# Kernel optimization log

Hardware: AMD Instinct MI355X
Metric: run time of the kernel (lower is better)

The kernel has to match this reference:

```python
import jax, jax.numpy as jnp
import numpy as np

B, S, D, H = 4, 2048, 1024, 16
HD = D // H


def setup_inputs() -> dict:
    key = jax.random.key(0)
    k1, k2, k3 = jax.random.split(key, 3)
    x = jax.random.normal(k1, (B, S, D), dtype=jnp.float32)
    # xavier-ish scaling for stable softmax
    W_attn = jax.random.normal(k2, (3 * D, D), dtype=jnp.float32) * (1.0 / np.sqrt(2 * D))
    b_attn = jnp.zeros((3 * D,), dtype=jnp.float32)
    W_out = jax.random.normal(k3, (D, D), dtype=jnp.float32) * (1.0 / np.sqrt(D))
    b_out = jnp.zeros((D,), dtype=jnp.float32)
    return {"x": x, "W_attn": W_attn, "b_attn": b_attn, "W_out": W_out, "b_out": b_out}


def reference(x, W_attn, b_attn, W_out, b_out):
    bs, seq, d = x.shape
    # fused QKV projection (torch Linear: y = x @ W.T + b)
    kqv = jnp.einsum("bsd,ed->bse", x, W_attn) + b_attn
    # NOTE: source splits as k, q, v (k first)
    k, q, v = jnp.split(kqv, 3, axis=2)
    # [b, s, h, hd] -> [b, h, s, hd]
    k = k.reshape(bs, seq, H, HD).transpose(0, 2, 1, 3)
    q = q.reshape(bs, seq, H, HD).transpose(0, 2, 1, 3)
    v = v.reshape(bs, seq, H, HD).transpose(0, 2, 1, 3)
    scale = 1.0 / np.sqrt(HD)
    scores = jnp.einsum("bhqd,bhkd->bhqk", q, k) * scale
    attn = jax.nn.softmax(scores, axis=-1)
    y = jnp.einsum("bhqk,bhkd->bhqd", attn, v)
    y = y.transpose(0, 2, 1, 3).reshape(bs, seq, d)
    out = jnp.einsum("bsd,ed->bse", y, W_out) + b_out
    return out
```

## Files before the change

### kernel.cpp

```cpp
#include <hip/hip_runtime.h>

typedef unsigned short u16;
typedef unsigned int u32;
typedef __attribute__((ext_vector_type(2))) u32 u32x2;
typedef __attribute__((ext_vector_type(4))) u32 u32x4;
typedef __attribute__((ext_vector_type(8))) short bf16x8;
typedef __attribute__((ext_vector_type(4))) short bf16x4;
typedef __attribute__((ext_vector_type(4))) float f32x4;

__device__ __forceinline__ u16 f2bf(float f) {
  u32 b = __float_as_uint(f);
  b += 0x7fffu + ((b >> 16) & 1u);
  return (u16)(b >> 16);
}

__device__ __forceinline__ u32 pk2bf(float a, float b) {
#if __has_builtin(__builtin_amdgcn_cvt_pk_bf16_f32)
  return __builtin_bit_cast(u32, __builtin_amdgcn_cvt_pk_bf16_f32(a, b));
#else
  return (u32)f2bf(a) | ((u32)f2bf(b) << 16);
#endif
}

__device__ __forceinline__ bf16x8 mk_ones8() {
  u32x4 t;
  t[0] = t[1] = t[2] = t[3] = 0x3F803F80u;
  return __builtin_bit_cast(bf16x8, t);
}

__device__ __forceinline__ float fexp2(float x) {
#if __has_builtin(__builtin_amdgcn_exp2f)
  return __builtin_amdgcn_exp2f(x);
#else
  return exp2f(x);
#endif
}

__device__ __forceinline__ void gload_lds16(const u16* g, u16* l) {
  __builtin_amdgcn_global_load_lds((const __attribute__((address_space(1))) void*)g,
                                   (__attribute__((address_space(3))) void*)l, 16, 0, 0);
}

__global__ __launch_bounds__(256) void cvt_f32_bf16(const float* __restrict__ in,
                                                    u16* __restrict__ out) {
  long i = ((long)blockIdx.x * 256 + threadIdx.x) * 8;
  u32 u[8];
#pragma unroll
  for (int j = 0; j < 8; j++) {
    u32 b = __float_as_uint(in[i + j]);
    u[j] = (b + 0x7fffu + ((b >> 16) & 1u)) >> 16;
  }
  u32x4 o;
  o[0] = u[0] | (u[1] << 16);
  o[1] = u[2] | (u[3] << 16);
  o[2] = u[4] | (u[5] << 16);
  o[3] = u[6] | (u[7] << 16);
  *(u32x4*)(out + i) = o;
}

__device__ __forceinline__ void gemm_core_128(const u16* __restrict__ A,
                                              const u16* __restrict__ B, int K,
                                              int m0, int n0, u16* As, u16* Bs,
                                              f32x4 acc[4][4]) {
  int t = threadIdx.x;
  int lane = t & 63, w = t >> 6;
  int quad = lane >> 4, l16 = lane & 15;
  int wm = (w >> 1) * 64, wn = (w & 1) * 64;
  int lr = lane >> 3, lc = lane & 7;
  int cg = lc ^ lr;
  int swz = l16 & 7;
  for (int k0 = 0; k0 < K; k0 += 64) {
#pragma unroll
    for (int i = 0; i < 4; i++) {
      int r0 = i * 32 + w * 8;
      gload_lds16(&A[(long)(m0 + r0 + lr) * K + k0 + cg * 8], &As[r0 * 64]);
      gload_lds16(&B[(long)(n0 + r0 + lr) * K + k0 + cg * 8], &Bs[r0 * 64]);
    }
    __syncthreads();
#pragma unroll
    for (int ks = 0; ks < 2; ks++) {
      bf16x8 a[4], b[4];
#pragma unroll
      for (int tm = 0; tm < 4; tm++)
        a[tm] = *(const bf16x8*)&As[(wm + tm * 16 + l16) * 64 + ((ks * 4 + quad) ^ swz) * 8];
#pragma unroll
      for (int tn = 0; tn < 4; tn++)
        b[tn] = *(const bf16x8*)&Bs[(wn + tn * 16 + l16) * 64 + ((ks * 4 + quad) ^ swz) * 8];
#pragma unroll
      for (int tm = 0; tm < 4; tm++)
#pragma unroll
        for (int tn = 0; tn < 4; tn++)
          acc[tm][tn] = __builtin_amdgcn_mfma_f32_16x16x32_bf16(a[tm], b[tn],
                                                                acc[tm][tn], 0, 0, 0);
    }
    __syncthreads();
  }
}

#define QSCALE 0.1803368801f
__global__ __launch_bounds__(256) void gemm_qkv(const u16* __restrict__ A,
                                                const u16* __restrict__ B,
                                                const float* __restrict__ bias,
                                                u16* __restrict__ Kg,
                                                u16* __restrict__ Qg,
                                                u16* __restrict__ Vg) {
  __shared__ __align__(16) u16 As[128 * 64];
  __shared__ __align__(16) u16 Bs[128 * 64];
  const int K = 1024;
  int m0 = blockIdx.y * 128, n0 = blockIdx.x * 128;
  f32x4 acc[4][4];
#pragma unroll
  for (int i = 0; i < 4; i++)
#pragma unroll
    for (int j = 0; j < 4; j++) acc[i][j] = (f32x4)0.0f;
  gemm_core_128(A, B, K, m0, n0, As, Bs, acc);

  int t = threadIdx.x, lane = t & 63, w = t >> 6;
  int quad = lane >> 4, l16 = lane & 15;
  int wm = (w >> 1) * 64, wn = (w & 1) * 64;
#pragma unroll
  for (int tn = 0; tn < 4; tn++) {
    int n = n0 + wn + tn * 16 + l16;
    float bv = bias[n];
    int which = n >> 10;
    int h = (n >> 6) & 15, d = n & 63;
#pragma unroll
    for (int tm = 0; tm < 4; tm++) {
      int m = m0 + wm + tm * 16 + quad * 4;
      int b = m >> 11, s = m & 2047;
      long bh = (long)b * 16 + h;
      if (which == 2) {
        u32x2 pk;
        pk[0] = pk2bf(acc[tm][tn][0] + bv, acc[tm][tn][1] + bv);
        pk[1] = pk2bf(acc[tm][tn][2] + bv, acc[tm][tn][3] + bv);
        *(u32x2*)&Vg[(bh * 64 + d) * 2048 + s] = pk;
      } else {
#pragma unroll
        for (int r = 0; r < 4; r++) {
          float v = acc[tm][tn][r] + bv;
          if (which == 0)
            Kg[(bh * 2048 + s + r) * 64 + d] = f2bf(v);
          else
            Qg[(bh * 2048 + s + r) * 64 + d] = f2bf(v * QSCALE);
        }
      }
    }
  }
}

__global__ __launch_bounds__(256) void gemm_out(const u16* __restrict__ A,
                                                const u16* __restrict__ B,
                                                const float* __restrict__ bias,
                                                float* __restrict__ out) {
  __shared__ __align__(16) u16 As[128 * 64];
  __shared__ __align__(16) u16 Bs[128 * 64];
  const int K = 1024, N = 1024;
  int m0 = blockIdx.y * 128, n0 = blockIdx.x * 128;
  f32x4 acc[4][4];
#pragma unroll
  for (int i = 0; i < 4; i++)
#pragma unroll
    for (int j = 0; j < 4; j++) acc[i][j] = (f32x4)0.0f;
  gemm_core_128(A, B, K, m0, n0, As, Bs, acc);

  int t = threadIdx.x, lane = t & 63, w = t >> 6;
  int quad = lane >> 4, l16 = lane & 15;
  int wm = (w >> 1) * 64, wn = (w & 1) * 64;
#pragma unroll
  for (int tn = 0; tn < 4; tn++) {
    int n = n0 + wn + tn * 16 + l16;
    float bv = bias[n];
#pragma unroll
    for (int tm = 0; tm < 4; tm++) {
#pragma unroll
      for (int r = 0; r < 4; r++) {
        int m = m0 + wm + tm * 16 + quad * 4 + r;
        out[(long)m * N + n] = acc[tm][tn][r] + bv;
      }
    }
  }
}

#define SYNC                                       \
  __builtin_amdgcn_sched_barrier(0);               \
  asm volatile("s_waitcnt vmcnt(0)" ::: "memory"); \
  __builtin_amdgcn_s_barrier();                    \
  __builtin_amdgcn_sched_barrier(0)

#define STAGE_KV(tt, bb)                                      \
  do {                                                        \
    gload_lds16(Kst + (long)(tt)*4096, &Ks[bb][w * 8 * 64]);  \
    gload_lds16(Vst + (tt)*64, &Vs[bb][w * 8 * 64]);          \
  } while (0)

#define COMPUTE(bb)                                                            \
  do {                                                                         \
    bf16x8 pf_[2][2];                                                          \
    _Pragma("unroll") for (int tq = 0; tq < 2; tq++) {                         \
      f32x4 s_[4];                                                             \
      __builtin_amdgcn_s_setprio(1);                                           \
      _Pragma("unroll") for (int tn = 0; tn < 4; tn++) {                       \
        bf16x8 kf0 = *(const bf16x8*)(kL0 + (bb)*4096 + tn * 1024);            \
        bf16x8 kf1 = *(const bf16x8*)(kL1 + (bb)*4096 + tn * 1024);            \
        s_[tn] = __builtin_amdgcn_mfma_f32_16x16x32_bf16(kf0, qf[tq][0], Z,    \
                                                         0, 0, 0);             \
        s_[tn] = __builtin_amdgcn_mfma_f32_16x16x32_bf16(kf1, qf[tq][1],       \
                                                         s_[tn], 0, 0, 0);     \
      }                                                                        \
      __builtin_amdgcn_s_setprio(0);                                           \
      _Pragma("unroll") for (int tn = 0; tn < 4; tn++) {                       \
        float e0 = fexp2(s_[tn][0]);                                           \
        float e1 = fexp2(s_[tn][1]);                                           \
        float e2 = fexp2(s_[tn][2]);                                           \
        float e3 = fexp2(s_[tn][3]);                                           \
        u32x2 pk;                                                              \
        pk[0] = pk2bf(e0, e1);                                                 \
        pk[1] = pk2bf(e2, e3);                                                 \
        *(u32x2*)(pW + tq * 1024 + woff[tn]) = pk;                             \
      }                                                                        \
    }                                                                          \
    _Pragma("unroll") for (int ks = 0; ks < 2; ks++)                           \
        _Pragma("unroll") for (int tq = 0; tq < 2; tq++) {                     \
      u32x2 lo = *(const u32x2*)(pR + tq * 1024 + prlo[ks]);                   \
      u32x2 hi = *(const u32x2*)(pR + tq * 1024 + prhi[ks]);                   \
      u32x4 cc;                                                                \
      cc[0] = lo[0];                                                           \
      cc[1] = lo[1];                                                           \
      cc[2] = hi[0];                                                           \
      cc[3] = hi[1];                                                           \
      pf_[tq][ks] = __builtin_bit_cast(bf16x8, cc);                            \
    }                                                                          \
    __builtin_amdgcn_s_setprio(1);                                             \
    _Pragma("unroll") for (int ks = 0; ks < 2; ks++) {                         \
      acc_sum[0] = __builtin_amdgcn_mfma_f32_16x16x32_bf16(ONES, pf_[0][ks],   \
                                                           acc_sum[0], 0, 0, 0); \
      acc_sum[1] = __builtin_amdgcn_mfma_f32_16x16x32_bf16(ONES, pf_[1][ks],   \
                                                           acc_sum[1], 0, 0, 0); \
      _Pragma("unroll") for (int dt = 0; dt < 4; dt++) {                       \
        bf16x8 vf = *(const bf16x8*)(vL[ks] + (bb)*4096 + dt * 1024);          \
        acc[dt][0] = __builtin_amdgcn_mfma_f32_16x16x32_bf16(vf, pf_[0][ks],   \
                                                             acc[dt][0], 0, 0, 0); \
        acc[dt][1] = __builtin_amdgcn_mfma_f32_16x16x32_bf16(vf, pf_[1][ks],   \
                                                             acc[dt][1], 0, 0, 0); \
      }                                                                        \
    }                                                                          \
    __builtin_amdgcn_s_setprio(0);                                             \
  } while (0)

__global__ __launch_bounds__(512, 4) void attn_kernel(const u16* __restrict__ Qg,
                                                      const u16* __restrict__ Kg,
                                                      const u16* __restrict__ Vg,
                                                      u16* __restrict__ Y) {
  __shared__ __align__(16) u16 Ks[2][64 * 64];
  __shared__ __align__(16) u16 Vs[2][64 * 64];
  __shared__ __align__(16) u16 Ps[8 * 32 * 64];
  int t = threadIdx.x, lane = t & 63, w = t >> 6;
  int quad = lane >> 4, l16 = lane & 15;
  int bh = blockIdx.y;
  int q0 = blockIdx.x * 256 + w * 32;
  int lr = lane >> 3, lc = lane & 7, cg = lc ^ lr;
  int swz = l16 & 7;
  u16* Pw = Ps + w * 2048;

  bf16x8 qf[2][2];
#pragma unroll
  for (int tq = 0; tq < 2; tq++) {
    const u16* qp = Qg + ((long)bh * 2048 + q0 + tq * 16 + l16) * 64;
    qf[tq][0] = *(const bf16x8*)(qp + quad * 8);
    qf[tq][1] = *(const bf16x8*)(qp + 32 + quad * 8);
  }

  const f32x4 Z = {0.0f, 0.0f, 0.0f, 0.0f};
  const bf16x8 ONES = mk_ones8();

  f32x4 acc[4][2];
  f32x4 acc_sum[2];
#pragma unroll
  for (int dt = 0; dt < 4; dt++)
#pragma unroll
    for (int tq = 0; tq < 2; tq++) acc[dt][tq] = (f32x4)0.0f;
  acc_sum[0] = (f32x4)0.0f;
  acc_sum[1] = (f32x4)0.0f;

  const u16* kL0 = &Ks[0][l16 * 64 + (quad ^ swz) * 8];
  const u16* kL1 = &Ks[0][l16 * 64 + ((4 + quad) ^ swz) * 8];
  const u16* vL[2] = {&Vs[0][l16 * 64 + (quad ^ swz) * 8],
                      &Vs[0][l16 * 64 + ((4 + quad) ^ swz) * 8]};
  u16* pW = Pw + l16 * 64;
  const u16* pR = Pw + l16 * 64;
  int woff[4], prlo[2], prhi[2];
#pragma unroll
  for (int tn = 0; tn < 4; tn++) woff[tn] = ((tn * 4 + quad) ^ l16) * 4;
#pragma unroll
  for (int ks = 0; ks < 2; ks++) {
    prlo[ks] = ((ks * 8 + quad * 2) ^ l16) * 4;
    prhi[ks] = ((ks * 8 + quad * 2 + 1) ^ l16) * 4;
  }

  const u16* Kst = Kg + ((long)bh * 2048 + w * 8 + lr) * 64 + cg * 8;
  const u16* Vst = Vg + ((long)(bh * 64 + w * 8 + lr)) * 2048 + cg * 8;

  STAGE_KV(0, 0);
  for (int tt = 0; tt < 30; tt += 2) {
    SYNC;
    STAGE_KV(tt + 1, 1);
    COMPUTE(0);
    SYNC;
    STAGE_KV(tt + 2, 0);
    COMPUTE(1);
  }
  SYNC;
  STAGE_KV(31, 1);
  COMPUTE(0);
  SYNC;
  COMPUTE(1);

  int b = bh >> 4, h = bh & 15;
#pragma unroll
  for (int tq = 0; tq < 2; tq++) {
    float inv = 1.0f / acc_sum[tq][0];
    long row = (long)b * 2048 + q0 + tq * 16 + l16;
#pragma unroll
    for (int dt = 0; dt < 4; dt++) {
      u32x2 pk;
      pk[0] = pk2bf(acc[dt][tq][0] * inv, acc[dt][tq][1] * inv);
      pk[1] = pk2bf(acc[dt][tq][2] * inv, acc[dt][tq][3] * inv);
      *(u32x2*)&Y[row * 1024 + h * 64 + dt * 16 + quad * 4] = pk;
    }
  }
}

extern "C" void kernel_launch(void* const* d_in, const int* in_sizes, int n_in,
                              void* d_out, int out_size, void* d_ws, size_t ws_size,
                              hipStream_t stream) {
  const float* x = (const float*)d_in[0];
  const float* W_attn = (const float*)d_in[1];
  const float* b_attn = (const float*)d_in[2];
  const float* W_out = (const float*)d_in[3];
  const float* b_out = (const float*)d_in[4];
  float* out = (float*)d_out;

  char* ws = (char*)d_ws;
  u16* xb = (u16*)ws;
  u16* Wab = (u16*)(ws + 16777216);
  u16* Wob = (u16*)(ws + 16777216 + 6291456);
  u16* Kg = (u16*)(ws + 25165824);
  u16* Qg = Kg + 8388608;
  u16* Vg = Qg + 8388608;
  u16* Yb = xb;

  cvt_f32_bf16<<<4096, 256, 0, stream>>>(x, xb);
  cvt_f32_bf16<<<1536, 256, 0, stream>>>(W_attn, Wab);
  cvt_f32_bf16<<<512, 256, 0, stream>>>(W_out, Wob);

  gemm_qkv<<<dim3(24, 64), 256, 0, stream>>>(xb, Wab, b_attn, Kg, Qg, Vg);
  attn_kernel<<<dim3(8, 64), 512, 0, stream>>>(Qg, Kg, Vg, Yb);
  gemm_out<<<dim3(8, 64), 256, 0, stream>>>(Yb, Wob, b_out, out);
}
```

Baseline: 292.7 us.

## Split attention KV tile across wave pairs with LDS reduction; fuse conversion kernels

The attention kernel now uses 256-thread blocks covering 64 queries instead of 512 threads covering 256 queries, launching four times as many blocks. Within each block, pairs of waves split each 64-key tile's columns and merge their partial outputs and row sums through LDS at the end. This is meant to raise the block count for better CU occupancy and load balance, at the cost of loading K/V four times more often per head and adding an epilogue reduction. The three f32-to-bf16 conversion launches are also merged into one kernel to cut launch overhead.

After: 287.4 us. No clear change (-1.8%).

```diff
diff --git a/kernel.cpp b/kernel.cpp
--- a/kernel.cpp
+++ b/kernel.cpp
@@ -5,7 +5,6 @@
 typedef __attribute__((ext_vector_type(2))) u32 u32x2;
 typedef __attribute__((ext_vector_type(4))) u32 u32x4;
 typedef __attribute__((ext_vector_type(8))) short bf16x8;
-typedef __attribute__((ext_vector_type(4))) short bf16x4;
 typedef __attribute__((ext_vector_type(4))) float f32x4;
 
 __device__ __forceinline__ u16 f2bf(float f) {
@@ -36,14 +35,33 @@
 #endif
 }
 
+__device__ __forceinline__ f32x4 mfma32(bf16x8 a, bf16x8 b, f32x4 c) {
+  return __builtin_amdgcn_mfma_f32_16x16x32_bf16(a, b, c, 0, 0, 0);
+}
+
 __device__ __forceinline__ void gload_lds16(const u16* g, u16* l) {
   __builtin_amdgcn_global_load_lds((const __attribute__((address_space(1))) void*)g,
                                    (__attribute__((address_space(3))) void*)l, 16, 0, 0);
 }
 
-__global__ __launch_bounds__(256) void cvt_f32_bf16(const float* __restrict__ in,
-                                                    u16* __restrict__ out) {
-  long i = ((long)blockIdx.x * 256 + threadIdx.x) * 8;
+__global__ __launch_bounds__(256) void cvt_all(const float* __restrict__ x,
+                                               const float* __restrict__ wa,
+                                               const float* __restrict__ wo,
+                                               u16* __restrict__ xb,
+                                               u16* __restrict__ wab,
+                                               u16* __restrict__ wob) {
+  int blk = blockIdx.x;
+  const float* in;
+  u16* out;
+  long base;
+  if (blk < 4096) {
+    in = x; out = xb; base = blk;
+  } else if (blk < 5632) {
+    in = wa; out = wab; base = blk - 4096;
+  } else {
+    in = wo; out = wob; base = blk - 5632;
+  }
+  long i = (base * 256 + threadIdx.x) * 8;
   u32 u[8];
 #pragma unroll
   for (int j = 0; j < 8; j++) {
@@ -187,28 +205,31 @@
   __builtin_amdgcn_s_barrier();                    \
   __builtin_amdgcn_sched_barrier(0)
 
-#define STAGE_KV(tt, bb)                                      \
-  do {                                                        \
-    gload_lds16(Kst + (long)(tt)*4096, &Ks[bb][w * 8 * 64]);  \
-    gload_lds16(Vst + (tt)*64, &Vs[bb][w * 8 * 64]);          \
+#define STAGE_KV(tt, bb)                                                       \
+  do {                                                                         \
+    gload_lds16(Kst + (long)(tt)*4096, Ks0 + (bb)*4096 + w * 1024);            \
+    gload_lds16(Kst + (long)(tt)*4096 + 512, Ks0 + (bb)*4096 + w * 1024 + 512);\
+    gload_lds16(Vst + (tt)*64, Vs0 + (bb)*4096 + w * 1024);                    \
+    gload_lds16(Vst + (tt)*64 + 8 * 2048, Vs0 + (bb)*4096 + w * 1024 + 512);   \
   } while (0)
 
 #define COMPUTE(bb)                                                            \
   do {                                                                         \
-    bf16x8 pf_[2][2];                                                          \
+    bf16x8 kf_[2][2];                                                          \
+    _Pragma("unroll") for (int tn = 0; tn < 2; tn++) {                         \
+      kf_[tn][0] = *(const bf16x8*)(kL0 + (bb)*4096 + tn * 1024);              \
+      kf_[tn][1] = *(const bf16x8*)(kL1 + (bb)*4096 + tn * 1024);              \
+    }                                                                          \
+    bf16x8 pf_[2];                                                             \
     _Pragma("unroll") for (int tq = 0; tq < 2; tq++) {                         \
-      f32x4 s_[4];                                                             \
+      f32x4 s_[2];                                                             \
       __builtin_amdgcn_s_setprio(1);                                           \
-      _Pragma("unroll") for (int tn = 0; tn < 4; tn++) {                       \
-        bf16x8 kf0 = *(const bf16x8*)(kL0 + (bb)*4096 + tn * 1024);            \
-        bf16x8 kf1 = *(const bf16x8*)(kL1 + (bb)*4096 + tn * 1024);            \
-        s_[tn] = __builtin_amdgcn_mfma_f32_16x16x32_bf16(kf0, qf[tq][0], Z,    \
-                                                         0, 0, 0);             \
-        s_[tn] = __builtin_amdgcn_mfma_f32_16x16x32_bf16(kf1, qf[tq][1],       \
-                                                         s_[tn], 0, 0, 0);     \
+      _Pragma("unroll") for (int tn = 0; tn < 2; tn++) {                       \
+        s_[tn] = mfma32(kf_[tn][0], qf[tq][0], Z);                             \
+        s_[tn] = mfma32(kf_[tn][1], qf[tq][1], s_[tn]);                        \
       }                                                                        \
       __builtin_amdgcn_s_setprio(0);                                           \
-      _Pragma("unroll") for (int tn = 0; tn < 4; tn++) {                       \
+      _Pragma("unroll") for (int tn = 0; tn < 2; tn++) {                       \
         float e0 = fexp2(s_[tn][0]);                                           \
         float e1 = fexp2(s_[tn][1]);                                           \
         float e2 = fexp2(s_[tn][2]);                                           \
@@ -216,51 +237,46 @@
         u32x2 pk;                                                              \
         pk[0] = pk2bf(e0, e1);                                                 \
         pk[1] = pk2bf(e2, e3);                                                 \
-        *(u32x2*)(pW + tq * 1024 + woff[tn]) = pk;                             \
+        *(u32x2*)(pW + tq * 512 + woff[tn]) = pk;                              \
       }                                                                        \
     }                                                                          \
-    _Pragma("unroll") for (int ks = 0; ks < 2; ks++)                           \
-        _Pragma("unroll") for (int tq = 0; tq < 2; tq++) {                     \
-      u32x2 lo = *(const u32x2*)(pR + tq * 1024 + prlo[ks]);                   \
-      u32x2 hi = *(const u32x2*)(pR + tq * 1024 + prhi[ks]);                   \
+    _Pragma("unroll") for (int tq = 0; tq < 2; tq++) {                         \
+      u32x2 lo = *(const u32x2*)(pR + tq * 512 + prlo);                        \
+      u32x2 hi = *(const u32x2*)(pR + tq * 512 + prhi);                        \
       u32x4 cc;                                                                \
       cc[0] = lo[0];                                                           \
       cc[1] = lo[1];                                                           \
       cc[2] = hi[0];                                                           \
       cc[3] = hi[1];                                                           \
-      pf_[tq][ks] = __builtin_bit_cast(bf16x8, cc);                            \
+      pf_[tq] = __builtin_bit_cast(bf16x8, cc);                                \
     }                                                                          \
     __builtin_amdgcn_s_setprio(1);                                             \
-    _Pragma("unroll") for (int ks = 0; ks < 2; ks++) {                         \
-      acc_sum[0] = __builtin_amdgcn_mfma_f32_16x16x32_bf16(ONES, pf_[0][ks],   \
-                                                           acc_sum[0], 0, 0, 0); \
-      acc_sum[1] = __builtin_amdgcn_mfma_f32_16x16x32_bf16(ONES, pf_[1][ks],   \
-                                                           acc_sum[1], 0, 0, 0); \
-      _Pragma("unroll") for (int dt = 0; dt < 4; dt++) {                       \
-        bf16x8 vf = *(const bf16x8*)(vL[ks] + (bb)*4096 + dt * 1024);          \
-        acc[dt][0] = __builtin_amdgcn_mfma_f32_16x16x32_bf16(vf, pf_[0][ks],   \
-                                                             acc[dt][0], 0, 0, 0); \
-        acc[dt][1] = __builtin_amdgcn_mfma_f32_16x16x32_bf16(vf, pf_[1][ks],   \
-                                                             acc[dt][1], 0, 0, 0); \
-      }                                                                        \
+    acc_sum[0] = mfma32(ONES, pf_[0], acc_sum[0]);                             \
+    acc_sum[1] = mfma32(ONES, pf_[1], acc_sum[1]);                             \
+    _Pragma("unroll") for (int dt = 0; dt < 4; dt++) {                         \
+      bf16x8 vf = *(const bf16x8*)(vL + (bb)*4096 + dt * 1024);                \
+      acc[dt][0] = mfma32(vf, pf_[0], acc[dt][0]);                             \
+      acc[dt][1] = mfma32(vf, pf_[1], acc[dt][1]);                             \
     }                                                                          \
     __builtin_amdgcn_s_setprio(0);                                             \
   } while (0)
 
-__global__ __launch_bounds__(512, 4) void attn_kernel(const u16* __restrict__ Qg,
+__global__ __launch_bounds__(256, 4) void attn_kernel(const u16* __restrict__ Qg,
                                                       const u16* __restrict__ Kg,
                                                       const u16* __restrict__ Vg,
                                                       u16* __restrict__ Y) {
-  __shared__ __align__(16) u16 Ks[2][64 * 64];
-  __shared__ __align__(16) u16 Vs[2][64 * 64];
-  __shared__ __align__(16) u16 Ps[8 * 32 * 64];
+  __shared__ __align__(16) u16 lds[20480];
+  u16* Ks0 = lds;
+  u16* Vs0 = lds + 8192;
+  u16* Ps0 = lds + 16384;
+
   int t = threadIdx.x, lane = t & 63, w = t >> 6;
   int quad = lane >> 4, l16 = lane & 15;
+  int p = w >> 1, kvh = w & 1;
   int bh = blockIdx.y;
-  int q0 = blockIdx.x * 256 + w * 32;
+  int q0 = blockIdx.x * 64 + p * 32;
   int lr = lane >> 3, lc = lane & 7, cg = lc ^ lr;
   int swz = l16 & 7;
-  u16* Pw = Ps + w * 2048;
 
   bf16x8 qf[2][2];
 #pragma unroll
@@ -282,23 +298,19 @@
   acc_sum[0] = (f32x4)0.0f;
   acc_sum[1] = (f32x4)0.0f;
 
-  const u16* kL0 = &Ks[0][l16 * 64 + (quad ^ swz) * 8];
-  const u16* kL1 = &Ks[0][l16 * 64 + ((4 + quad) ^ swz) * 8];
-  const u16* vL[2] = {&Vs[0][l16 * 64 + (quad ^ swz) * 8],
-                      &Vs[0][l16 * 64 + ((4 + quad) ^ swz) * 8]};
-  u16* pW = Pw + l16 * 64;
-  const u16* pR = Pw + l16 * 64;
-  int woff[4], prlo[2], prhi[2];
-#pragma unroll
-  for (int tn = 0; tn < 4; tn++) woff[tn] = ((tn * 4 + quad) ^ l16) * 4;
-#pragma unroll
-  for (int ks = 0; ks < 2; ks++) {
-    prlo[ks] = ((ks * 8 + quad * 2) ^ l16) * 4;
-    prhi[ks] = ((ks * 8 + quad * 2 + 1) ^ l16) * 4;
-  }
-
-  const u16* Kst = Kg + ((long)bh * 2048 + w * 8 + lr) * 64 + cg * 8;
-  const u16* Vst = Vg + ((long)(bh * 64 + w * 8 + lr)) * 2048 + cg * 8;
+  const u16* kL0 = Ks0 + (kvh * 32 + l16) * 64 + (quad ^ swz) * 8;
+  const u16* kL1 = Ks0 + (kvh * 32 + l16) * 64 + ((4 + quad) ^ swz) * 8;
+  const u16* vL = Vs0 + l16 * 64 + ((kvh * 4 + quad) ^ swz) * 8;
+  u16* pW = Ps0 + w * 1024 + l16 * 32;
+  const u16* pR = pW;
+  int woff[2];
+#pragma unroll
+  for (int tn = 0; tn < 2; tn++) woff[tn] = ((tn * 4 + quad) ^ swz) * 4;
+  int prlo = ((quad * 2) ^ swz) * 4;
+  int prhi = ((quad * 2 + 1) ^ swz) * 4;
+
+  const u16* Kst = Kg + ((long)bh * 2048 + w * 16 + lr) * 64 + cg * 8;
+  const u16* Vst = Vg + ((long)(bh * 64 + w * 16 + lr)) * 2048 + cg * 8;
 
   STAGE_KV(0, 0);
   for (int tt = 0; tt < 30; tt += 2) {
@@ -315,17 +327,35 @@
   SYNC;
   COMPUTE(1);
 
-  int b = bh >> 4, h = bh & 15;
-#pragma unroll
-  for (int tq = 0; tq < 2; tq++) {
-    float inv = 1.0f / acc_sum[tq][0];
-    long row = (long)b * 2048 + q0 + tq * 16 + l16;
-#pragma unroll
-    for (int dt = 0; dt < 4; dt++) {
-      u32x2 pk;
-      pk[0] = pk2bf(acc[dt][tq][0] * inv, acc[dt][tq][1] * inv);
-      pk[1] = pk2bf(acc[dt][tq][2] * inv, acc[dt][tq][3] * inv);
-      *(u32x2*)&Y[row * 1024 + h * 64 + dt * 16 + quad * 4] = pk;
+  __syncthreads();
+  float* red = (float*)lds;
+  int slot = (p * 64 + lane) * 44;
+  if (kvh) {
+#pragma unroll
+    for (int dt = 0; dt < 4; dt++)
+#pragma unroll
+      for (int tq = 0; tq < 2; tq++)
+        *(f32x4*)(red + slot + (dt * 2 + tq) * 4) = acc[dt][tq];
+    red[slot + 32] = acc_sum[0][0];
+    red[slot + 33] = acc_sum[1][0];
+  }
+  __syncthreads();
+  if (!kvh) {
+    float s0 = acc_sum[0][0] + red[slot + 32];
+    float s1 = acc_sum[1][0] + red[slot + 33];
+    float inv[2] = {1.0f / s0, 1.0f / s1};
+    int b = bh >> 4, h = bh & 15;
+#pragma unroll
+    for (int tq = 0; tq < 2; tq++) {
+      long row = (long)b * 2048 + q0 + tq * 16 + l16;
+#pragma unroll
+      for (int dt = 0; dt < 4; dt++) {
+        f32x4 a = acc[dt][tq] + *(const f32x4*)(red + slot + (dt * 2 + tq) * 4);
+        u32x2 pk;
+        pk[0] = pk2bf(a[0] * inv[tq], a[1] * inv[tq]);
+        pk[1] = pk2bf(a[2] * inv[tq], a[3] * inv[tq]);
+        *(u32x2*)&Y[row * 1024 + h * 64 + dt * 16 + quad * 4] = pk;
+      }
     }
   }
 }
@@ -349,11 +379,9 @@
   u16* Vg = Qg + 8388608;
   u16* Yb = xb;
 
-  cvt_f32_bf16<<<4096, 256, 0, stream>>>(x, xb);
-  cvt_f32_bf16<<<1536, 256, 0, stream>>>(W_attn, Wab);
-  cvt_f32_bf16<<<512, 256, 0, stream>>>(W_out, Wob);
+  cvt_all<<<6144, 256, 0, stream>>>(x, W_attn, W_out, xb, Wab, Wob);
 
   gemm_qkv<<<dim3(24, 64), 256, 0, stream>>>(xb, Wab, b_attn, Kg, Qg, Vg);
-  attn_kernel<<<dim3(8, 64), 512, 0, stream>>>(Qg, Kg, Vg, Yb);
+  attn_kernel<<<dim3(32, 64), 256, 0, stream>>>(Qg, Kg, Vg, Yb);
   gemm_out<<<dim3(8, 64), 256, 0, stream>>>(Yb, Wob, b_out, out);
 }
```

## Swap GEMM operand roles for vectorized epilogue stores and merge conversion kernels

Applied to the files above, without the earlier changes.

Both projection GEMMs now treat the weight matrix as the A operand and the activations as B, so the output tile is transposed. Each lane's four accumulator rows then map to contiguous feature indices, which allows packed 8-byte bf16 stores for K and Q and 16-byte float4 stores for the final output instead of scattered scalar stores. The V store turns into scalar strided writes, and the grid dimensions are swapped to match. The three fp32-to-bf16 conversion launches are also merged into one kernel to save launch overhead.

Result: faster. 278.3 us (-4.9%).

```diff
diff --git a/kernel.cpp b/kernel.cpp
--- a/kernel.cpp
+++ b/kernel.cpp
@@ -5,7 +5,6 @@
 typedef __attribute__((ext_vector_type(2))) u32 u32x2;
 typedef __attribute__((ext_vector_type(4))) u32 u32x4;
 typedef __attribute__((ext_vector_type(8))) short bf16x8;
-typedef __attribute__((ext_vector_type(4))) short bf16x4;
 typedef __attribute__((ext_vector_type(4))) float f32x4;
 
 __device__ __forceinline__ u16 f2bf(float f) {
@@ -41,9 +40,24 @@
                                    (__attribute__((address_space(3))) void*)l, 16, 0, 0);
 }
 
-__global__ __launch_bounds__(256) void cvt_f32_bf16(const float* __restrict__ in,
-                                                    u16* __restrict__ out) {
-  long i = ((long)blockIdx.x * 256 + threadIdx.x) * 8;
+__global__ __launch_bounds__(256) void cvt_all(const float* __restrict__ x,
+                                               const float* __restrict__ wa,
+                                               const float* __restrict__ wo,
+                                               u16* __restrict__ xb,
+                                               u16* __restrict__ wab,
+                                               u16* __restrict__ wob) {
+  int blk = blockIdx.x;
+  const float* in;
+  u16* out;
+  long base;
+  if (blk < 4096) {
+    in = x; out = xb; base = blk;
+  } else if (blk < 5632) {
+    in = wa; out = wab; base = blk - 4096;
+  } else {
+    in = wo; out = wob; base = blk - 5632;
+  }
+  long i = (base * 256 + threadIdx.x) * 8;
   u32 u[8];
 #pragma unroll
   for (int j = 0; j < 8; j++) {
@@ -118,31 +132,33 @@
   int t = threadIdx.x, lane = t & 63, w = t >> 6;
   int quad = lane >> 4, l16 = lane & 15;
   int wm = (w >> 1) * 64, wn = (w & 1) * 64;
-#pragma unroll
-  for (int tn = 0; tn < 4; tn++) {
-    int n = n0 + wn + tn * 16 + l16;
-    float bv = bias[n];
-    int which = n >> 10;
-    int h = (n >> 6) & 15, d = n & 63;
-#pragma unroll
-    for (int tm = 0; tm < 4; tm++) {
-      int m = m0 + wm + tm * 16 + quad * 4;
-      int b = m >> 11, s = m & 2047;
+  int which = m0 >> 10;
+#pragma unroll
+  for (int tm = 0; tm < 4; tm++) {
+    int m = m0 + wm + tm * 16 + quad * 4;
+    int h = (m >> 6) & 15, d0 = m & 63;
+    f32x4 b4 = *(const f32x4*)&bias[m];
+#pragma unroll
+    for (int tn = 0; tn < 4; tn++) {
+      int n = n0 + wn + tn * 16 + l16;
+      int b = n >> 11, s = n & 2047;
       long bh = (long)b * 16 + h;
-      if (which == 2) {
+      if (which == 0) {
         u32x2 pk;
-        pk[0] = pk2bf(acc[tm][tn][0] + bv, acc[tm][tn][1] + bv);
-        pk[1] = pk2bf(acc[tm][tn][2] + bv, acc[tm][tn][3] + bv);
-        *(u32x2*)&Vg[(bh * 64 + d) * 2048 + s] = pk;
+        pk[0] = pk2bf(acc[tm][tn][0] + b4[0], acc[tm][tn][1] + b4[1]);
+        pk[1] = pk2bf(acc[tm][tn][2] + b4[2], acc[tm][tn][3] + b4[3]);
+        *(u32x2*)&Kg[(bh * 2048 + s) * 64 + d0] = pk;
+      } else if (which == 1) {
+        u32x2 pk;
+        pk[0] = pk2bf((acc[tm][tn][0] + b4[0]) * QSCALE,
+                      (acc[tm][tn][1] + b4[1]) * QSCALE);
+        pk[1] = pk2bf((acc[tm][tn][2] + b4[2]) * QSCALE,
+                      (acc[tm][tn][3] + b4[3]) * QSCALE);
+        *(u32x2*)&Qg[(bh * 2048 + s) * 64 + d0] = pk;
       } else {
 #pragma unroll
-        for (int r = 0; r < 4; r++) {
-          float v = acc[tm][tn][r] + bv;
-          if (which == 0)
-            Kg[(bh * 2048 + s + r) * 64 + d] = f2bf(v);
-          else
-            Qg[(bh * 2048 + s + r) * 64 + d] = f2bf(v * QSCALE);
-        }
+        for (int r = 0; r < 4; r++)
+          Vg[(bh * 64 + d0 + r) * 2048 + s] = f2bf(acc[tm][tn][r] + b4[r]);
       }
     }
   }
@@ -154,7 +170,7 @@
                                                 float* __restrict__ out) {
   __shared__ __align__(16) u16 As[128 * 64];
   __shared__ __align__(16) u16 Bs[128 * 64];
-  const int K = 1024, N = 1024;
+  const int K = 1024;
   int m0 = blockIdx.y * 128, n0 = blockIdx.x * 128;
   f32x4 acc[4][4];
 #pragma unroll
@@ -167,16 +183,14 @@
   int quad = lane >> 4, l16 = lane & 15;
   int wm = (w >> 1) * 64, wn = (w & 1) * 64;
 #pragma unroll
-  for (int tn = 0; tn < 4; tn++) {
-    int n = n0 + wn + tn * 16 + l16;
-    float bv = bias[n];
-#pragma unroll
-    for (int tm = 0; tm < 4; tm++) {
-#pragma unroll
-      for (int r = 0; r < 4; r++) {
-        int m = m0 + wm + tm * 16 + quad * 4 + r;
-        out[(long)m * N + n] = acc[tm][tn][r] + bv;
-      }
+  for (int tm = 0; tm < 4; tm++) {
+    int m = m0 + wm + tm * 16 + quad * 4;
+    f32x4 b4 = *(const f32x4*)&bias[m];
+#pragma unroll
+    for (int tn = 0; tn < 4; tn++) {
+      int n = n0 + wn + tn * 16 + l16;
+      f32x4 o = acc[tm][tn] + b4;
+      *(f32x4*)&out[(long)n * 1024 + m] = o;
     }
   }
 }
@@ -349,11 +363,9 @@
   u16* Vg = Qg + 8388608;
   u16* Yb = xb;
 
-  cvt_f32_bf16<<<4096, 256, 0, stream>>>(x, xb);
-  cvt_f32_bf16<<<1536, 256, 0, stream>>>(W_attn, Wab);
-  cvt_f32_bf16<<<512, 256, 0, stream>>>(W_out, Wob);
-
-  gemm_qkv<<<dim3(24, 64), 256, 0, stream>>>(xb, Wab, b_attn, Kg, Qg, Vg);
+  cvt_all<<<6144, 256, 0, stream>>>(x, W_attn, W_out, xb, Wab, Wob);
+
+  gemm_qkv<<<dim3(64, 24), 256, 0, stream>>>(Wab, xb, b_attn, Kg, Qg, Vg);
   attn_kernel<<<dim3(8, 64), 512, 0, stream>>>(Qg, Kg, Vg, Yb);
-  gemm_out<<<dim3(8, 64), 256, 0, stream>>>(Yb, Wob, b_out, out);
-}
+  gemm_out<<<dim3(64, 8), 256, 0, stream>>>(Wob, Yb, b_out, out);
+}
```
